# Kernel optimization log

Hardware: AMD Instinct MI355X
Metric: run time of the kernel (lower is better)

The kernel has to match this reference:

```python
import jax, jax.numpy as jnp
import numpy as np

SLOW = 32      # LSTM hidden size per weight-neuron
MSG = 16       # message size
MICRO = 2      # micro ticks per layer per step
LAYERS = [(256, 128), (128, 64)]
OUT_IDX = 0
EPS = 1e-6


def _lstm(x, h, c, Wi, Wh, b):
    g = x @ Wi + h @ Wh + b
    i, f, gg, o = jnp.split(g, 4, axis=-1)
    c = jax.nn.sigmoid(f) * c + jax.nn.sigmoid(i) * jnp.tanh(gg)
    h = jax.nn.sigmoid(o) * jnp.tanh(c)
    return h, c


def _ln(x, s, b):
    m = x.mean(-1, keepdims=True)
    v = ((x - m) ** 2).mean(-1, keepdims=True)
    return (x - m) * jax.lax.rsqrt(v + EPS) * s + b


def _merge(state):
    # mean-reduce first half of channels over batch, broadcast back
    half = state.shape[-1] // 2
    s1, s2 = state[..., :half], state[..., half:]
    s1 = jnp.broadcast_to(s1.mean(axis=0, keepdims=True), s1.shape)
    return jnp.concatenate([s1, s2], axis=-1)


def setup_inputs() -> dict:
    key = jax.random.key(0)
    ks = jax.random.split(key, 8)
    T, B = 4, 8
    sc = 0.1
    return {
        "inputs": jax.random.normal(ks[0], (T, B, LAYERS[0][0]), jnp.float32),
        "labels": jax.random.randint(ks[1], (T, B), 0, LAYERS[-1][1]),
        "Wi": jax.random.normal(ks[2], (2 * MSG, 4 * SLOW), jnp.float32) * sc,
        "Wh": jax.random.normal(ks[3], (SLOW, 4 * SLOW), jnp.float32) * sc,
        "b_lstm": jnp.zeros((4 * SLOW,), jnp.float32),
        "Wf": jax.random.normal(ks[4], (SLOW, MSG), jnp.float32) * sc,
        "bf": jnp.zeros((MSG,), jnp.float32),
        "Wb": jax.random.normal(ks[5], (SLOW, MSG), jnp.float32) * sc,
        "bwb": jnp.zeros((MSG,), jnp.float32),
        "ln_fs": jnp.ones((MSG,), jnp.float32),
        "ln_fb": jnp.zeros((MSG,), jnp.float32),
        "ln_bs": jnp.ones((MSG,), jnp.float32),
        "ln_bb": jnp.zeros((MSG,), jnp.float32),
    }


def reference(inputs, labels, Wi, Wh, b_lstm, Wf, bf, Wb, bwb,
              ln_fs, ln_fb, ln_bs, ln_bb):
    T, B, _ = inputs.shape
    n_out = LAYERS[-1][1]
    onehot = jax.nn.one_hot(labels, n_out, dtype=inputs.dtype)

    hs0 = tuple(jnp.zeros((B, i, o, SLOW), inputs.dtype) for i, o in LAYERS)
    cs0 = tuple(jnp.zeros((B, i, o, SLOW), inputs.dtype) for i, o in LAYERS)
    fwd0 = tuple(jnp.zeros((B, i, MSG), inputs.dtype) for i, o in LAYERS)
    bwd0 = tuple(jnp.zeros((B, o, MSG), inputs.dtype) for i, o in LAYERS)
    err0 = jnp.zeros((B, n_out, 2), inputs.dtype)

    def layer(h, c, f, bd):
        # h,c: (B,i,o,S); f: (B,i,M); bd: (B,o,M)
        Bq, ni, no, _ = h.shape
        x = jnp.concatenate([
            jnp.broadcast_to(f[:, :, None, :], (Bq, ni, no, MSG)),
            jnp.broadcast_to(bd[:, None, :, :], (Bq, ni, no, MSG)),
        ], axis=-1)  # (B,i,o,2M)
        for _ in range(MICRO):
            h, c = _lstm(x, h, c, Wi, Wh, b_lstm)
        fm = _ln(h @ Wf + bf, ln_fs, ln_fb)   # (B,i,o,M)
        bm = _ln(h @ Wb + bwb, ln_bs, ln_bb)  # (B,i,o,M)
        return h, c, fm.mean(axis=1), bm.mean(axis=2)

    def step(carry, x):
        hs, cs, fwd, bwd, error = carry
        inp, oh = x
        hs = [_merge(h) for h in hs]
        cs = [_merge(c) for c in cs]
        fwd = list(fwd)
        bwd = list(bwd)
        # inject input into channel 0 of first layer fwd msg
        fwd[0] = jnp.pad(inp[..., None], ((0, 0), (0, 0), (0, MSG - 1)))
        # inject 2-channel error into last layer bwd msg
        bwd[-1] = jnp.pad(error, ((0, 0), (0, 0), (0, MSG - 2)))
        out = None
        for i in range(len(LAYERS)):
            h, c, nf, nb = layer(hs[i], cs[i], fwd[i], bwd[i])
            hs[i], cs[i] = h, c
            if i > 0:
                bwd[i - 1] = nb.reshape(bwd[i - 1].shape)
            if i < len(LAYERS) - 1:
                fwd[i + 1] = nf.reshape(fwd[i + 1].shape)
            else:
                out = nf[..., OUT_IDX]  # (B, n_out)
        grad = jax.nn.softmax(out, axis=-1) - oh  # cross-entropy grad
        new_error = jnp.stack([grad, oh], axis=-1)  # feed_label=True
        return (tuple(hs), tuple(cs), tuple(fwd), tuple(bwd), new_error), out

    carry = (hs0, cs0, fwd0, bwd0, err0)
    _, outputs = jax.lax.scan(step, carry, (inputs, onehot))
    return outputs  # (T, B, n_out)
```

## Files before the change

kernel.cpp:

```cpp
#include <hip/hip_runtime.h>
#include <hip/hip_bf16.h>

#define SLOW 32
#define MSG 16
#define TSTEPS 4
#define BATCH 8
#define NI0 256
#define NO0 128
#define NI1 128
#define NO1 64

typedef __bf16 bf16x8 __attribute__((ext_vector_type(8)));
typedef float f32x4 __attribute__((ext_vector_type(4)));

__device__ __forceinline__ float rcpf(float x) { return __builtin_amdgcn_rcpf(x); }
__device__ __forceinline__ float sigf(float x) { return rcpf(1.f + __expf(-x)); }
__device__ __forceinline__ float tanh_apx(float x) {
    float xc = fminf(fmaxf(x, -15.f), 15.f);
    float e = __expf(-2.f * xc);
    return (1.f - e) * rcpf(1.f + e);
}
__device__ __forceinline__ unsigned short f2bf(float x) {
    __bf16 h = (__bf16)x;
    return __builtin_bit_cast(unsigned short, h);
}
__device__ __forceinline__ float bf2f(unsigned short u) {
    __bf16 h = __builtin_bit_cast(__bf16, u);
    return (float)h;
}
__device__ __forceinline__ float sum16(float v) {
    v += __shfl_xor(v, 1); v += __shfl_xor(v, 2);
    v += __shfl_xor(v, 4); v += __shfl_xor(v, 8);
    return v;
}

__global__ void k_prep(const float* __restrict__ Wh, const float* __restrict__ Wf,
                       const float* __restrict__ Wb, const float* __restrict__ Wi,
                       unsigned short* __restrict__ WhBp,
                       unsigned short* __restrict__ WfBp,
                       unsigned short* __restrict__ WbBp,
                       unsigned short* __restrict__ WiFp) {
    int i = blockIdx.x * 256 + threadIdx.x;
    if (i < 4096) {
        int e = i & 7, l = (i >> 3) & 63, nt = i >> 9;
        int k = (l >> 4) * 8 + e, col = nt * 16 + (l & 15);
        WhBp[i] = f2bf(Wh[k * 128 + col]);
    } else if (i < 4608) {
        int j = i - 4096;
        int e = j & 7, l = j >> 3;
        int k = (l >> 4) * 8 + e;
        WfBp[j] = f2bf(Wf[k * 16 + (l & 15)]);
    } else if (i < 5120) {
        int j = i - 4608;
        int e = j & 7, l = j >> 3;
        int k = (l >> 4) * 8 + e;
        WbBp[j] = f2bf(Wb[k * 16 + (l & 15)]);
    } else if (i < 9216) {
        int j = i - 5120;
        int e = j & 7, l = (j >> 3) & 63, nt = j >> 9;
        int k = (l >> 4) * 8 + e, col = nt * 16 + (l & 15);
        WiFp[j] = (k < 16) ? f2bf(Wi[k * 128 + col]) : (unsigned short)0;
    }
}

__global__ __launch_bounds__(256) void k_l0(
    const float* __restrict__ inp, const float* __restrict__ Wi,
    const unsigned short* __restrict__ WhBp, const float* __restrict__ b_lstm,
    const unsigned short* __restrict__ WfBp, const float* __restrict__ bf_,
    const float* __restrict__ ln_fs, const float* __restrict__ ln_fb,
    unsigned short* __restrict__ h0bf, float* __restrict__ c0g,
    const float* __restrict__ nb1, float* __restrict__ nf_part, int t) {
    int q = blockIdx.x & 1;
    int no = (blockIdx.x >> 1) & 127;
    int b = blockIdx.x >> 8;
    int tid = threadIdx.x;
    int w = __builtin_amdgcn_readfirstlane(tid >> 6);
    int l = tid & 63, lo = l & 15, hg = l >> 4;
    const bool wb = (t < TSTEPS - 1);

    __shared__ unsigned short Hbf[128 * 40];
    __shared__ unsigned short BW[4096];
    __shared__ unsigned short BFr[512];
    __shared__ float gsh[128];
    __shared__ float mi_l[128];
    __shared__ float wi0[128];
    __shared__ float redn[4][16];

    {
        unsigned int* d = (unsigned int*)BW;
        const unsigned int* s = (const unsigned int*)WhBp;
#pragma unroll
        for (int i = tid; i < 2048; i += 256) d[i] = s[i];
        ((unsigned int*)BFr)[tid] = ((const unsigned int*)WfBp)[tid];
    }
    if (tid < 128) {
        float acc = b_lstm[tid];
        if (t > 0) {
            const float* nbr = nb1 + ((size_t)b * NO0 + no) * MSG;
#pragma unroll
            for (int m = 0; m < MSG; m++) acc += nbr[m] * Wi[(MSG + m) * 128 + tid];
        }
        gsh[tid] = acc;
        wi0[tid] = Wi[tid];
        mi_l[tid] = inp[((size_t)t * BATCH + b) * NI0 + q * 128 + tid];
    }
    {
        int lc = tid >> 1, half = tid & 1;
        unsigned int* hl = (unsigned int*)Hbf;
        if (t > 0) {
            const unsigned int* hsrc =
                (const unsigned int*)h0bf +
                ((size_t)(b * NO0 + no) * 256 + q * 128 + lc) * 16 + half * 8;
#pragma unroll
            for (int j = 0; j < 8; j++) hl[lc * 20 + half * 8 + j] = hsrc[j];
        } else {
#pragma unroll
            for (int j = 0; j < 8; j++) hl[lc * 20 + half * 8 + j] = 0u;
        }
    }
    size_t cbase = (size_t)(b * NO0 + no) * 256 * 32;
    float cst[2][4][2];
    if (t > 0) {
#pragma unroll
        for (int mi_ = 0; mi_ < 2; mi_++)
#pragma unroll
            for (int r = 0; r < 4; r++) {
                int gc = q * 128 + (w * 2 + mi_) * 16 + hg * 4 + r;
#pragma unroll
                for (int hi = 0; hi < 2; hi++)
                    cst[mi_][r][hi] = c0g[cbase + (size_t)gc * 32 + lo + 16 * hi];
            }
    } else {
#pragma unroll
        for (int mi_ = 0; mi_ < 2; mi_++)
#pragma unroll
            for (int r = 0; r < 4; r++) { cst[mi_][r][0] = 0.f; cst[mi_][r][1] = 0.f; }
    }
    __syncthreads();

    float g8[8], w8[8];
#pragma unroll
    for (int nt = 0; nt < 8; nt++) { g8[nt] = gsh[lo + 16 * nt]; w8[nt] = wi0[lo + 16 * nt]; }
    f32x4 miv[2];
#pragma unroll
    for (int mi_ = 0; mi_ < 2; mi_++)
#pragma unroll
        for (int r = 0; r < 4; r++)
            miv[mi_][r] = mi_l[(w * 2 + mi_) * 16 + hg * 4 + r];

#pragma unroll
    for (int micro = 0; micro < 2; micro++) {
#pragma unroll
        for (int mi_ = 0; mi_ < 2; mi_++) {
            int lt = w * 2 + mi_;
            bf16x8 A = *(const bf16x8*)&Hbf[(lt * 16 + lo) * 40 + hg * 8];
            f32x4 acc[4];
#pragma unroll
            for (int g = 0; g < 4; g++) {
                int nt = 2 * g;
                bf16x8 B = *(const bf16x8*)&BW[(nt * 64 + l) * 8];
                f32x4 ci = g8[nt] + miv[mi_] * w8[nt];
                acc[g] = __builtin_amdgcn_mfma_f32_16x16x32_bf16(A, B, ci, 0, 0, 0);
            }
#pragma unroll
            for (int r = 0; r < 4; r++) {
                int lrow = lt * 16 + hg * 4 + r;
                float cn = sigf(acc[1][r]) * cst[mi_][r][0] + sigf(acc[0][r]) * tanh_apx(acc[2][r]);
                cst[mi_][r][0] = cn;
                float hv = sigf(acc[3][r]) * tanh_apx(cn);
                Hbf[lrow * 40 + lo] = f2bf(hv);
                if (micro == 1 && wb)
                    c0g[cbase + (size_t)(q * 128 + lrow) * 32 + lo] = cn;
            }
#pragma unroll
            for (int g = 0; g < 4; g++) {
                int nt = 2 * g + 1;
                bf16x8 B = *(const bf16x8*)&BW[(nt * 64 + l) * 8];
                f32x4 ci = g8[nt] + miv[mi_] * w8[nt];
                acc[g] = __builtin_amdgcn_mfma_f32_16x16x32_bf16(A, B, ci, 0, 0, 0);
            }
#pragma unroll
            for (int r = 0; r < 4; r++) {
                int lrow = lt * 16 + hg * 4 + r;
                float cn = sigf(acc[1][r]) * cst[mi_][r][1] + sigf(acc[0][r]) * tanh_apx(acc[2][r]);
                cst[mi_][r][1] = cn;
                float hv = sigf(acc[3][r]) * tanh_apx(cn);
                Hbf[lrow * 40 + lo + 16] = f2bf(hv);
                if (micro == 1 && wb)
                    c0g[cbase + (size_t)(q * 128 + lrow) * 32 + lo + 16] = cn;
            }
        }
    }

    bf16x8 Ff = *(const bf16x8*)&BFr[l * 8];
    float lnfs = ln_fs[lo], lnfb = ln_fb[lo];
    float bfv = bf_[lo];
    f32x4 cif = {bfv, bfv, bfv, bfv};
    float nfp = 0.f;
#pragma unroll
    for (int mi_ = 0; mi_ < 2; mi_++) {
        int lt = w * 2 + mi_;
        bf16x8 A = *(const bf16x8*)&Hbf[(lt * 16 + lo) * 40 + hg * 8];
        f32x4 f = __builtin_amdgcn_mfma_f32_16x16x32_bf16(A, Ff, cif, 0, 0, 0);
#pragma unroll
        for (int r = 0; r < 4; r++) {
            float x = f[r];
            float mean = sum16(x) * 0.0625f;
            float d = x - mean;
            float rs = rsqrtf(sum16(d * d) * 0.0625f + 1e-6f);
            nfp += d * rs * lnfs + lnfb;
        }
    }
    nfp += __shfl_xor(nfp, 16);
    nfp += __shfl_xor(nfp, 32);
    if (l < 16) redn[w][l] = nfp;
    __syncthreads();
    if (tid < 16)
        nf_part[(((size_t)b * NO0 + no) * 2 + q) * 16 + tid] =
            redn[0][tid] + redn[1][tid] + redn[2][tid] + redn[3][tid];

    if (wb) {
        int lc = tid >> 1, part = tid & 1;
        unsigned int* hdst =
            (unsigned int*)h0bf +
            ((size_t)(b * NO0 + no) * 256 + q * 128 + lc) * 16 + part * 8;
        const unsigned int* hl = (const unsigned int*)Hbf;
#pragma unroll
        for (int j = 0; j < 8; j++) hdst[j] = hl[lc * 20 + part * 8 + j];
    }
}

__global__ __launch_bounds__(256) void k_l1(
    const float* __restrict__ Wi, const unsigned short* __restrict__ WhBp,
    const float* __restrict__ b_lstm,
    const unsigned short* __restrict__ WfBp, const float* __restrict__ bf_,
    const float* __restrict__ ln_fs, const float* __restrict__ ln_fb,
    const unsigned short* __restrict__ WbBp, const float* __restrict__ bwb,
    const float* __restrict__ ln_bs, const float* __restrict__ ln_bb,
    const unsigned short* __restrict__ WiFp,
    unsigned short* __restrict__ h1bf, float* __restrict__ c1g,
    const float* __restrict__ nf_part, const float* __restrict__ gradP,
    const float* __restrict__ ohP,
    float* __restrict__ bm_g, float* __restrict__ outsum_part, int t) {
    int q = blockIdx.x & 1;
    int no = (blockIdx.x >> 1) & 63;
    int b = blockIdx.x >> 7;
    int tid = threadIdx.x;
    int w = __builtin_amdgcn_readfirstlane(tid >> 6);
    int l = tid & 63, lo = l & 15, hg = l >> 4;
    const bool wb = (t < TSTEPS - 1);

    __shared__ unsigned short Hbf[64 * 40];
    __shared__ unsigned short BW[4096];
    __shared__ unsigned short WiF[4096];
    __shared__ unsigned short BFr[512];
    __shared__ unsigned short BBr[512];
    __shared__ float gsh[128];
    __shared__ float red[4];

    {
        unsigned int* d = (unsigned int*)BW;
        const unsigned int* s = (const unsigned int*)WhBp;
        unsigned int* d2 = (unsigned int*)WiF;
        const unsigned int* s2 = (const unsigned int*)WiFp;
#pragma unroll
        for (int i = tid; i < 2048; i += 256) { d[i] = s[i]; d2[i] = s2[i]; }
        ((unsigned int*)BFr)[tid] = ((const unsigned int*)WfBp)[tid];
        ((unsigned int*)BBr)[tid] = ((const unsigned int*)WbBp)[tid];
    }
    if (tid < 128) {
        float acc = b_lstm[tid];
        if (t > 0) {
            float g = gradP[b * NO1 + no], oh = ohP[b * NO1 + no];
            acc += g * Wi[MSG * 128 + tid] + oh * Wi[(MSG + 1) * 128 + tid];
        }
        gsh[tid] = acc;
    }
    {
        int lc = tid >> 2, part = tid & 3;
        unsigned int* hl = (unsigned int*)Hbf;
        if (t > 0) {
            const unsigned int* hsrc =
                (const unsigned int*)h1bf +
                ((size_t)(b * NO1 + no) * 128 + q * 64 + lc) * 16 + part * 4;
#pragma unroll
            for (int j = 0; j < 4; j++) hl[lc * 20 + part * 4 + j] = hsrc[j];
        } else {
#pragma unroll
            for (int j = 0; j < 4; j++) hl[lc * 20 + part * 4 + j] = 0u;
        }
    }
    size_t cbase = (size_t)(b * NO1 + no) * 128 * 32;
    float cst[4][2];
    if (t > 0) {
#pragma unroll
        for (int r = 0; r < 4; r++) {
            int gc = q * 64 + w * 16 + hg * 4 + r;
#pragma unroll
            for (int hi = 0; hi < 2; hi++)
                cst[r][hi] = c1g[cbase + (size_t)gc * 32 + lo + 16 * hi];
        }
    } else {
#pragma unroll
        for (int r = 0; r < 4; r++) { cst[r][0] = 0.f; cst[r][1] = 0.f; }
    }
    bf16x8 Anf;
#pragma unroll
    for (int e = 0; e < 8; e++) Anf[e] = (__bf16)0.f;
    if (hg < 2) {
        const float* p = nf_part +
            ((size_t)b * 128 + q * 64 + w * 16 + lo) * 32 + hg * 8;
#pragma unroll
        for (int e = 0; e < 8; e++)
            Anf[e] = (__bf16)((p[e] + p[e + 16]) * (1.f / 256.f));
    }
    __syncthreads();

    f32x4 xf4[8];
    {
        f32x4 zz = {0.f, 0.f, 0.f, 0.f};
#pragma unroll
        for (int nt = 0; nt < 8; nt++) {
            bf16x8 B = *(const bf16x8*)&WiF[(nt * 64 + l) * 8];
            xf4[nt] = __builtin_amdgcn_mfma_f32_16x16x32_bf16(Anf, B, zz, 0, 0, 0);
        }
    }
    float g8[8];
#pragma unroll
    for (int nt = 0; nt < 8; nt++) g8[nt] = gsh[lo + 16 * nt];

#pragma unroll
    for (int micro = 0; micro < 2; micro++) {
        bf16x8 A = *(const bf16x8*)&Hbf[(w * 16 + lo) * 40 + hg * 8];
        f32x4 acc[4];
#pragma unroll
        for (int g = 0; g < 4; g++) {
            int nt = 2 * g;
            bf16x8 B = *(const bf16x8*)&BW[(nt * 64 + l) * 8];
            f32x4 ci = xf4[nt] + g8[nt];
            acc[g] = __builtin_amdgcn_mfma_f32_16x16x32_bf16(A, B, ci, 0, 0, 0);
        }
#pragma unroll
        for (int r = 0; r < 4; r++) {
            float cn = sigf(acc[1][r]) * cst[r][0] + sigf(acc[0][r]) * tanh_apx(acc[2][r]);
            cst[r][0] = cn;
            float hv = sigf(acc[3][r]) * tanh_apx(cn);
            Hbf[(w * 16 + hg * 4 + r) * 40 + lo] = f2bf(hv);
            if (micro == 1 && wb)
                c1g[cbase + (size_t)(q * 64 + w * 16 + hg * 4 + r) * 32 + lo] = cn;
        }
#pragma unroll
        for (int g = 0; g < 4; g++) {
            int nt = 2 * g + 1;
            bf16x8 B = *(const bf16x8*)&BW[(nt * 64 + l) * 8];
            f32x4 ci = xf4[nt] + g8[nt];
            acc[g] = __builtin_amdgcn_mfma_f32_16x16x32_bf16(A, B, ci, 0, 0, 0);
        }
#pragma unroll
        for (int r = 0; r < 4; r++) {
            float cn = sigf(acc[1][r]) * cst[r][1] + sigf(acc[0][r]) * tanh_apx(acc[2][r]);
            cst[r][1] = cn;
            float hv = sigf(acc[3][r]) * tanh_apx(cn);
            Hbf[(w * 16 + hg * 4 + r) * 40 + lo + 16] = f2bf(hv);
            if (micro == 1 && wb)
                c1g[cbase + (size_t)(q * 64 + w * 16 + hg * 4 + r) * 32 + lo + 16] = cn;
        }
    }

    bf16x8 Ff = *(const bf16x8*)&BFr[l * 8];
    float lnfs = ln_fs[lo], lnfb = ln_fb[lo];
    float bfv = bf_[lo];
    f32x4 cif = {bfv, bfv, bfv, bfv};
    float op = 0.f;
    {
        bf16x8 A = *(const bf16x8*)&Hbf[(w * 16 + lo) * 40 + hg * 8];
        f32x4 f = __builtin_amdgcn_mfma_f32_16x16x32_bf16(A, Ff, cif, 0, 0, 0);
#pragma unroll
        for (int r = 0; r < 4; r++) {
            float x = f[r];
            float mean = sum16(x) * 0.0625f;
            float d = x - mean;
            float rs = rsqrtf(sum16(d * d) * 0.0625f + 1e-6f);
            op += d * rs * lnfs + lnfb;
        }
        if (wb) {
            bf16x8 Bb = *(const bf16x8*)&BBr[l * 8];
            float lnbs = ln_bs[lo], lnbb = ln_bb[lo];
            float bwv = bwb[lo];
            f32x4 cib = {bwv, bwv, bwv, bwv};
            f32x4 g = __builtin_amdgcn_mfma_f32_16x16x32_bf16(A, Bb, cib, 0, 0, 0);
#pragma unroll
            for (int r = 0; r < 4; r++) {
                int gc = q * 64 + w * 16 + hg * 4 + r;
                float x = g[r];
                float mean = sum16(x) * 0.0625f;
                float d = x - mean;
                float rs = rsqrtf(sum16(d * d) * 0.0625f + 1e-6f);
                bm_g[(((size_t)b * NO1 + no) * MSG + lo) * NI1 + gc] = d * rs * lnbs + lnbb;
            }
        }
    }
    op += __shfl_xor(op, 16);
    op += __shfl_xor(op, 32);
    if (l == 0) red[w] = op;
    __syncthreads();
    if (tid == 0)
        outsum_part[((size_t)b * NO1 + no) * 2 + q] = red[0] + red[1] + red[2] + red[3];

    if (wb) {
        int lc = tid >> 2, part = tid & 3;
        unsigned int* hdst =
            (unsigned int*)h1bf +
            ((size_t)(b * NO1 + no) * 128 + q * 64 + lc) * 16 + part * 4;
        const unsigned int* hl = (const unsigned int*)Hbf;
#pragma unroll
        for (int j = 0; j < 4; j++) hdst[j] = hl[lc * 20 + part * 4 + j];
    }
}

__global__ __launch_bounds__(256) void k_step_end(
    unsigned int* __restrict__ h0, float* __restrict__ c0,
    unsigned int* __restrict__ h1, float* __restrict__ c1,
    const float* __restrict__ bm_g, float* __restrict__ nb1,
    const float* __restrict__ outsum_part, const int* __restrict__ labels,
    float* __restrict__ dout, float* __restrict__ gradP,
    float* __restrict__ ohP, int t) {
    int bid = blockIdx.x;
    if (bid < 1920) {
        int idx = bid * 256 + threadIdx.x;
        if (idx < 262144) {
            int u = idx & 7, cell = (idx >> 3) & 255, no = idx >> 11;
            size_t base = ((size_t)no * 256 + cell) * 16 + u;
            const size_t strd = (size_t)128 * 256 * 16;
            float s0 = 0.f, s1 = 0.f;
#pragma unroll
            for (int b = 0; b < 8; b++) {
                unsigned int v = h0[base + b * strd];
                s0 += bf2f((unsigned short)(v & 0xffff));
                s1 += bf2f((unsigned short)(v >> 16));
            }
            unsigned int mv = (unsigned int)f2bf(s0 * 0.125f) |
                              ((unsigned int)f2bf(s1 * 0.125f) << 16);
#pragma unroll
            for (int b = 0; b < 8; b++) h0[base + b * strd] = mv;
            return;
        }
        idx -= 262144;
        if (idx < 131072) {
            int s4 = idx & 3, cell = (idx >> 2) & 255, no = idx >> 10;
            float4* C = (float4*)c0;
            size_t base = ((size_t)no * 256 + cell) * 8 + s4;
            const size_t strd = (size_t)128 * 256 * 8;
            float4 a = {0.f, 0.f, 0.f, 0.f};
#pragma unroll
            for (int b = 0; b < 8; b++) {
                float4 v = C[base + b * strd];
                a.x += v.x; a.y += v.y; a.z += v.z; a.w += v.w;
            }
            a.x *= 0.125f; a.y *= 0.125f; a.z *= 0.125f; a.w *= 0.125f;
#pragma unroll
            for (int b = 0; b < 8; b++) C[base + b * strd] = a;
            return;
        }
        idx -= 131072;
        if (idx < 65536) {
            int u = idx & 7, cell = (idx >> 3) & 127, no = idx >> 10;
            size_t base = ((size_t)no * 128 + cell) * 16 + u;
            const size_t strd = (size_t)64 * 128 * 16;
            float s0 = 0.f, s1 = 0.f;
#pragma unroll
            for (int b = 0; b < 8; b++) {
                unsigned int v = h1[base + b * strd];
                s0 += bf2f((unsigned short)(v & 0xffff));
                s1 += bf2f((unsigned short)(v >> 16));
            }
            unsigned int mv = (unsigned int)f2bf(s0 * 0.125f) |
                              ((unsigned int)f2bf(s1 * 0.125f) << 16);
#pragma unroll
            for (int b = 0; b < 8; b++) h1[base + b * strd] = mv;
            return;
        }
        idx -= 65536;
        {
            int s4 = idx & 3, cell = (idx >> 2) & 127, no = idx >> 9;
            float4* C = (float4*)c1;
            size_t base = ((size_t)no * 128 + cell) * 8 + s4;
            const size_t strd = (size_t)64 * 128 * 8;
            float4 a = {0.f, 0.f, 0.f, 0.f};
#pragma unroll
            for (int b = 0; b < 8; b++) {
                float4 v = C[base + b * strd];
                a.x += v.x; a.y += v.y; a.z += v.z; a.w += v.w;
            }
            a.x *= 0.125f; a.y *= 0.125f; a.z *= 0.125f; a.w *= 0.125f;
#pragma unroll
            for (int b = 0; b < 8; b++) C[base + b * strd] = a;
        }
        return;
    }
    if (bid < 1984) {
        int g = (bid - 1920) * 256 + threadIdx.x;
        int ni = g & 127;
        int m = (g >> 7) & 15;
        int b = g >> 11;
        float a = 0.f;
#pragma unroll 8
        for (int no = 0; no < NO1; no++)
            a += bm_g[(((size_t)b * NO1 + no) * MSG + m) * NI1 + ni];
        nb1[((size_t)b * NI1 + ni) * MSG + m] = a * (1.f / NO1);
        return;
    }
    {
        int b = bid - 1984;
        int no = threadIdx.x;
        if (no < 64) {
            float v = (outsum_part[((size_t)b * NO1 + no) * 2] +
                       outsum_part[((size_t)b * NO1 + no) * 2 + 1]) * (1.f / 128.f);
            float mx = v;
#pragma unroll
            for (int d = 1; d < 64; d <<= 1) mx = fmaxf(mx, __shfl_xor(mx, d));
            float e = __expf(v - mx);
            float sum = e;
#pragma unroll
            for (int d = 1; d < 64; d <<= 1) sum += __shfl_xor(sum, d);
            int lbl = labels[t * BATCH + b];
            float oh = (no == lbl) ? 1.f : 0.f;
            gradP[b * NO1 + no] = e / sum - oh;
            ohP[b * NO1 + no] = oh;
            dout[((size_t)t * BATCH + b) * NO1 + no] = v;
        }
    }
}

__global__ void k_fin(const float* __restrict__ outsum_part,
                      float* __restrict__ dout) {
    int b = blockIdx.x;
    int no = threadIdx.x;
    float v = (outsum_part[((size_t)b * NO1 + no) * 2] +
               outsum_part[((size_t)b * NO1 + no) * 2 + 1]) * (1.f / 128.f);
    dout[((size_t)(TSTEPS - 1) * BATCH + b) * NO1 + no] = v;
}


extern "C" void kernel_launch(void* const* d_in, const int* in_sizes, int n_in,
                              void* d_out, int out_size, void* d_ws, size_t ws_size,
                              hipStream_t stream) {
    const float* inp   = (const float*)d_in[0];
    const int*   labels= (const int*)d_in[1];
    const float* Wi    = (const float*)d_in[2];
    const float* Wh    = (const float*)d_in[3];
    const float* b_lstm= (const float*)d_in[4];
    const float* Wf    = (const float*)d_in[5];
    const float* bf_   = (const float*)d_in[6];
    const float* Wb    = (const float*)d_in[7];
    const float* bwb   = (const float*)d_in[8];
    const float* ln_fs = (const float*)d_in[9];
    const float* ln_fb = (const float*)d_in[10];
    const float* ln_bs = (const float*)d_in[11];
    const float* ln_bb = (const float*)d_in[12];
    float* out = (float*)d_out;

    const size_t SZ0 = (size_t)BATCH * NO0 * 256 * 32;
    const size_t SZ1 = (size_t)BATCH * NO1 * 128 * 32;

    float* c0 = (float*)d_ws;
    float* c1 = c0 + SZ0;
    unsigned short* h0bf = (unsigned short*)(c1 + SZ1);
    unsigned short* h1bf = h0bf + SZ0;
    float* bm_g        = (float*)(h1bf + SZ1);
    float* nf_part     = bm_g + 1048576;
    float* nb1         = nf_part + 32768;
    float* outsum_part = nb1 + 16384;
    float* gradP       = outsum_part + 1024;
    float* ohP         = gradP + 512;
    unsigned short* WhBp = (unsigned short*)(ohP + 512);
    unsigned short* WfBp = WhBp + 4096;
    unsigned short* WbBp = WfBp + 512;
    unsigned short* WiFp = WbBp + 512;

    k_prep<<<36, 256, 0, stream>>>(Wh, Wf, Wb, Wi, WhBp, WfBp, WbBp, WiFp);

    for (int t = 0; t < TSTEPS; t++) {
        k_l0<<<BATCH * NO0 * 2, 256, 0, stream>>>(inp, Wi, WhBp, b_lstm, WfBp, bf_,
                                                  ln_fs, ln_fb, h0bf, c0, nb1,
                                                  nf_part, t);
        k_l1<<<BATCH * NO1 * 2, 256, 0, stream>>>(Wi, WhBp, b_lstm, WfBp, bf_,
                                                  ln_fs, ln_fb, WbBp, bwb, ln_bs, ln_bb,
                                                  WiFp, h1bf, c1, nf_part, gradP, ohP,
                                                  bm_g, outsum_part, t);
        if (t < TSTEPS - 1) {
            k_step_end<<<1992, 256, 0, stream>>>((unsigned int*)h0bf, c0,
                                                 (unsigned int*)h1bf, c1,
                                                 bm_g, nb1, outsum_part, labels,
                                                 out, gradP, ohP, t);
        } else {
            k_fin<<<BATCH, 64, 0, stream>>>(outsum_part, out);
        }
    }
}
```

Measured before the change: 279.6 us.

## Store batch-mean state compactly and fold layer-0 merge into layer-1 launch

The batch-mean merge no longer broadcasts averaged h/c back into all 8 batch copies. It writes a compact per-neuron mean buffer (hm/cm), which the LSTM kernels read for the first half of channels. The layer-0 merge reductions also move into extra blocks of the k_l1 launch, so they overlap with layer-1 compute and shrink k_step_end. This cuts the write-back traffic of the full state tensors, at the cost of extra workspace and a larger k_l1 grid.

```diff
diff --git a/kernel.cpp b/kernel.cpp
--- a/kernel.cpp
+++ b/kernel.cpp
@@ -69,6 +69,7 @@
     const unsigned short* __restrict__ WfBp, const float* __restrict__ bf_,
     const float* __restrict__ ln_fs, const float* __restrict__ ln_fb,
     unsigned short* __restrict__ h0bf, float* __restrict__ c0g,
+    const unsigned short* __restrict__ hm0, const float* __restrict__ cm0,
     const float* __restrict__ nb1, float* __restrict__ nf_part, int t) {
     int q = blockIdx.x & 1;
     int no = (blockIdx.x >> 1) & 127;
@@ -108,11 +109,17 @@
         int lc = tid >> 1, half = tid & 1;
         unsigned int* hl = (unsigned int*)Hbf;
         if (t > 0) {
-            const unsigned int* hsrc =
-                (const unsigned int*)h0bf +
-                ((size_t)(b * NO0 + no) * 256 + q * 128 + lc) * 16 + half * 8;
-#pragma unroll
-            for (int j = 0; j < 8; j++) hl[lc * 20 + half * 8 + j] = hsrc[j];
+            if (half == 0) {
+                const unsigned int* hsrc = (const unsigned int*)hm0 +
+                    ((size_t)no * 256 + q * 128 + lc) * 8;
+#pragma unroll
+                for (int j = 0; j < 8; j++) hl[lc * 20 + j] = hsrc[j];
+            } else {
+                const unsigned int* hsrc = (const unsigned int*)h0bf +
+                    ((size_t)(b * NO0 + no) * 256 + q * 128 + lc) * 16 + 8;
+#pragma unroll
+                for (int j = 0; j < 8; j++) hl[lc * 20 + 8 + j] = hsrc[j];
+            }
         } else {
 #pragma unroll
             for (int j = 0; j < 8; j++) hl[lc * 20 + half * 8 + j] = 0u;
@@ -126,9 +133,8 @@
 #pragma unroll
             for (int r = 0; r < 4; r++) {
                 int gc = q * 128 + (w * 2 + mi_) * 16 + hg * 4 + r;
-#pragma unroll
-                for (int hi = 0; hi < 2; hi++)
-                    cst[mi_][r][hi] = c0g[cbase + (size_t)gc * 32 + lo + 16 * hi];
+                cst[mi_][r][0] = cm0[((size_t)no * 256 + gc) * 16 + lo];
+                cst[mi_][r][1] = c0g[cbase + (size_t)gc * 32 + lo + 16];
             }
     } else {
 #pragma unroll
@@ -239,13 +245,51 @@
     const float* __restrict__ ln_bs, const float* __restrict__ ln_bb,
     const unsigned short* __restrict__ WiFp,
     unsigned short* __restrict__ h1bf, float* __restrict__ c1g,
+    const unsigned short* __restrict__ hm1, const float* __restrict__ cm1,
+    const unsigned short* __restrict__ h0bf, const float* __restrict__ c0g,
+    unsigned short* __restrict__ hm0, float* __restrict__ cm0,
     const float* __restrict__ nf_part, const float* __restrict__ gradP,
     const float* __restrict__ ohP,
     float* __restrict__ bm_g, float* __restrict__ outsum_part, int t) {
+    int tid = threadIdx.x;
+    if (blockIdx.x >= 1024) {
+        int mb = blockIdx.x - 1024;
+        if (mb < 1024) {
+            int idx = mb * 256 + tid;
+            int u = idx & 7, cell = (idx >> 3) & 255, no = idx >> 11;
+            size_t base = ((size_t)no * 256 + cell) * 16 + u;
+            const size_t strd = (size_t)NO0 * 256 * 16;
+            const unsigned int* H = (const unsigned int*)h0bf;
+            float s0 = 0.f, s1 = 0.f;
+#pragma unroll
+            for (int b = 0; b < 8; b++) {
+                unsigned int v = H[base + b * strd];
+                s0 += bf2f((unsigned short)(v & 0xffff));
+                s1 += bf2f((unsigned short)(v >> 16));
+            }
+            ((unsigned int*)hm0)[((size_t)no * 256 + cell) * 8 + u] =
+                (unsigned int)f2bf(s0 * 0.125f) | ((unsigned int)f2bf(s1 * 0.125f) << 16);
+        } else {
+            int idx = (mb - 1024) * 256 + tid;
+            int s4 = idx & 3, cell = (idx >> 2) & 255, no = idx >> 10;
+            const float4* C = (const float4*)c0g;
+            size_t base = ((size_t)no * 256 + cell) * 8 + s4;
+            const size_t strd = (size_t)NO0 * 256 * 8;
+            float4 a = {0.f, 0.f, 0.f, 0.f};
+#pragma unroll
+            for (int b = 0; b < 8; b++) {
+                float4 v = C[base + b * strd];
+                a.x += v.x; a.y += v.y; a.z += v.z; a.w += v.w;
+            }
+            a.x *= 0.125f; a.y *= 0.125f; a.z *= 0.125f; a.w *= 0.125f;
+            ((float4*)cm0)[((size_t)no * 256 + cell) * 4 + s4] = a;
+        }
+        return;
+    }
+
     int q = blockIdx.x & 1;
     int no = (blockIdx.x >> 1) & 63;
     int b = blockIdx.x >> 7;
-    int tid = threadIdx.x;
     int w = __builtin_amdgcn_readfirstlane(tid >> 6);
     int l = tid & 63, lo = l & 15, hg = l >> 4;
     const bool wb = (t < TSTEPS - 1);
@@ -280,11 +324,17 @@
         int lc = tid >> 2, part = tid & 3;
         unsigned int* hl = (unsigned int*)Hbf;
         if (t > 0) {
-            const unsigned int* hsrc =
-                (const unsigned int*)h1bf +
-                ((size_t)(b * NO1 + no) * 128 + q * 64 + lc) * 16 + part * 4;
-#pragma unroll
-            for (int j = 0; j < 4; j++) hl[lc * 20 + part * 4 + j] = hsrc[j];
+            if (part < 2) {
+                const unsigned int* hsrc = (const unsigned int*)hm1 +
+                    ((size_t)no * 128 + q * 64 + lc) * 8 + part * 4;
+#pragma unroll
+                for (int j = 0; j < 4; j++) hl[lc * 20 + part * 4 + j] = hsrc[j];
+            } else {
+                const unsigned int* hsrc = (const unsigned int*)h1bf +
+                    ((size_t)(b * NO1 + no) * 128 + q * 64 + lc) * 16 + part * 4;
+#pragma unroll
+                for (int j = 0; j < 4; j++) hl[lc * 20 + part * 4 + j] = hsrc[j];
+            }
         } else {
 #pragma unroll
             for (int j = 0; j < 4; j++) hl[lc * 20 + part * 4 + j] = 0u;
@@ -296,9 +346,8 @@
 #pragma unroll
         for (int r = 0; r < 4; r++) {
             int gc = q * 64 + w * 16 + hg * 4 + r;
-#pragma unroll
-            for (int hi = 0; hi < 2; hi++)
-                cst[r][hi] = c1g[cbase + (size_t)gc * 32 + lo + 16 * hi];
+            cst[r][0] = cm1[((size_t)no * 128 + gc) * 16 + lo];
+            cst[r][1] = c1g[cbase + (size_t)gc * 32 + lo + 16];
         }
     } else {
 #pragma unroll
@@ -419,87 +468,47 @@
 }
 
 __global__ __launch_bounds__(256) void k_step_end(
-    unsigned int* __restrict__ h0, float* __restrict__ c0,
-    unsigned int* __restrict__ h1, float* __restrict__ c1,
+    const unsigned int* __restrict__ h1, const float* __restrict__ c1,
+    unsigned short* __restrict__ hm1, float* __restrict__ cm1,
     const float* __restrict__ bm_g, float* __restrict__ nb1,
     const float* __restrict__ outsum_part, const int* __restrict__ labels,
     float* __restrict__ dout, float* __restrict__ gradP,
     float* __restrict__ ohP, int t) {
     int bid = blockIdx.x;
-    if (bid < 1920) {
+    if (bid < 256) {
         int idx = bid * 256 + threadIdx.x;
-        if (idx < 262144) {
-            int u = idx & 7, cell = (idx >> 3) & 255, no = idx >> 11;
-            size_t base = ((size_t)no * 256 + cell) * 16 + u;
-            const size_t strd = (size_t)128 * 256 * 16;
-            float s0 = 0.f, s1 = 0.f;
-#pragma unroll
-            for (int b = 0; b < 8; b++) {
-                unsigned int v = h0[base + b * strd];
-                s0 += bf2f((unsigned short)(v & 0xffff));
-                s1 += bf2f((unsigned short)(v >> 16));
-            }
-            unsigned int mv = (unsigned int)f2bf(s0 * 0.125f) |
-                              ((unsigned int)f2bf(s1 * 0.125f) << 16);
-#pragma unroll
-            for (int b = 0; b < 8; b++) h0[base + b * strd] = mv;
-            return;
-        }
-        idx -= 262144;
-        if (idx < 131072) {
-            int s4 = idx & 3, cell = (idx >> 2) & 255, no = idx >> 10;
-            float4* C = (float4*)c0;
-            size_t base = ((size_t)no * 256 + cell) * 8 + s4;
-            const size_t strd = (size_t)128 * 256 * 8;
-            float4 a = {0.f, 0.f, 0.f, 0.f};
-#pragma unroll
-            for (int b = 0; b < 8; b++) {
-                float4 v = C[base + b * strd];
-                a.x += v.x; a.y += v.y; a.z += v.z; a.w += v.w;
-            }
-            a.x *= 0.125f; a.y *= 0.125f; a.z *= 0.125f; a.w *= 0.125f;
-#pragma unroll
-            for (int b = 0; b < 8; b++) C[base + b * strd] = a;
-            return;
-        }
-        idx -= 131072;
-        if (idx < 65536) {
-            int u = idx & 7, cell = (idx >> 3) & 127, no = idx >> 10;
-            size_t base = ((size_t)no * 128 + cell) * 16 + u;
-            const size_t strd = (size_t)64 * 128 * 16;
-            float s0 = 0.f, s1 = 0.f;
-#pragma unroll
-            for (int b = 0; b < 8; b++) {
-                unsigned int v = h1[base + b * strd];
-                s0 += bf2f((unsigned short)(v & 0xffff));
-                s1 += bf2f((unsigned short)(v >> 16));
-            }
-            unsigned int mv = (unsigned int)f2bf(s0 * 0.125f) |
-                              ((unsigned int)f2bf(s1 * 0.125f) << 16);
-#pragma unroll
-            for (int b = 0; b < 8; b++) h1[base + b * strd] = mv;
-            return;
-        }
-        idx -= 65536;
-        {
-            int s4 = idx & 3, cell = (idx >> 2) & 127, no = idx >> 9;
-            float4* C = (float4*)c1;
-            size_t base = ((size_t)no * 128 + cell) * 8 + s4;
-            const size_t strd = (size_t)64 * 128 * 8;
-            float4 a = {0.f, 0.f, 0.f, 0.f};
-#pragma unroll
-            for (int b = 0; b < 8; b++) {
-                float4 v = C[base + b * strd];
-                a.x += v.x; a.y += v.y; a.z += v.z; a.w += v.w;
-            }
-            a.x *= 0.125f; a.y *= 0.125f; a.z *= 0.125f; a.w *= 0.125f;
-#pragma unroll
-            for (int b = 0; b < 8; b++) C[base + b * strd] = a;
-        }
+        int u = idx & 7, cell = (idx >> 3) & 127, no = idx >> 10;
+        size_t base = ((size_t)no * 128 + cell) * 16 + u;
+        const size_t strd = (size_t)NO1 * 128 * 16;
+        float s0 = 0.f, s1 = 0.f;
+#pragma unroll
+        for (int b = 0; b < 8; b++) {
+            unsigned int v = h1[base + b * strd];
+            s0 += bf2f((unsigned short)(v & 0xffff));
+            s1 += bf2f((unsigned short)(v >> 16));
+        }
+        ((unsigned int*)hm1)[((size_t)no * 128 + cell) * 8 + u] =
+            (unsigned int)f2bf(s0 * 0.125f) | ((unsigned int)f2bf(s1 * 0.125f) << 16);
         return;
     }
-    if (bid < 1984) {
-        int g = (bid - 1920) * 256 + threadIdx.x;
+    if (bid < 384) {
+        int idx = (bid - 256) * 256 + threadIdx.x;
+        int s4 = idx & 3, cell = (idx >> 2) & 127, no = idx >> 9;
+        const float4* C = (const float4*)c1;
+        size_t base = ((size_t)no * 128 + cell) * 8 + s4;
+        const size_t strd = (size_t)NO1 * 128 * 8;
+        float4 a = {0.f, 0.f, 0.f, 0.f};
+#pragma unroll
+        for (int b = 0; b < 8; b++) {
+            float4 v = C[base + b * strd];
+            a.x += v.x; a.y += v.y; a.z += v.z; a.w += v.w;
+        }
+        a.x *= 0.125f; a.y *= 0.125f; a.z *= 0.125f; a.w *= 0.125f;
+        ((float4*)cm1)[((size_t)no * 128 + cell) * 4 + s4] = a;
+        return;
+    }
+    if (bid < 448) {
+        int g = (bid - 384) * 256 + threadIdx.x;
         int ni = g & 127;
         int m = (g >> 7) & 15;
         int b = g >> 11;
@@ -511,7 +520,7 @@
         return;
     }
     {
-        int b = bid - 1984;
+        int b = bid - 448;
         int no = threadIdx.x;
         if (no < 64) {
             float v = (outsum_part[((size_t)b * NO1 + no) * 2] +
@@ -567,7 +576,11 @@
     float* c1 = c0 + SZ0;
     unsigned short* h0bf = (unsigned short*)(c1 + SZ1);
     unsigned short* h1bf = h0bf + SZ0;
-    float* bm_g        = (float*)(h1bf + SZ1);
+    float* cm0         = (float*)(h1bf + SZ1);
+    float* cm1         = cm0 + 524288;
+    unsigned short* hm0 = (unsigned short*)(cm1 + 131072);
+    unsigned short* hm1 = hm0 + 524288;
+    float* bm_g        = (float*)(hm1 + 131072);
     float* nf_part     = bm_g + 1048576;
     float* nb1         = nf_part + 32768;
     float* outsum_part = nb1 + 16384;
@@ -582,17 +595,19 @@
 
     for (int t = 0; t < TSTEPS; t++) {
         k_l0<<<BATCH * NO0 * 2, 256, 0, stream>>>(inp, Wi, WhBp, b_lstm, WfBp, bf_,
-                                                  ln_fs, ln_fb, h0bf, c0, nb1,
-                                                  nf_part, t);
-        k_l1<<<BATCH * NO1 * 2, 256, 0, stream>>>(Wi, WhBp, b_lstm, WfBp, bf_,
-                                                  ln_fs, ln_fb, WbBp, bwb, ln_bs, ln_bb,
-                                                  WiFp, h1bf, c1, nf_part, gradP, ohP,
-                                                  bm_g, outsum_part, t);
+                                                  ln_fs, ln_fb, h0bf, c0, hm0, cm0,
+                                                  nb1, nf_part, t);
+        int l1grid = (t < TSTEPS - 1) ? 2560 : 1024;
+        k_l1<<<l1grid, 256, 0, stream>>>(Wi, WhBp, b_lstm, WfBp, bf_,
+                                         ln_fs, ln_fb, WbBp, bwb, ln_bs, ln_bb,
+                                         WiFp, h1bf, c1, hm1, cm1,
+                                         h0bf, c0, hm0, cm0,
+                                         nf_part, gradP, ohP,
+                                         bm_g, outsum_part, t);
         if (t < TSTEPS - 1) {
-            k_step_end<<<1992, 256, 0, stream>>>((unsigned int*)h0bf, c0,
-                                                 (unsigned int*)h1bf, c1,
-                                                 bm_g, nb1, outsum_part, labels,
-                                                 out, gradP, ohP, t);
+            k_step_end<<<456, 256, 0, stream>>>((const unsigned int*)h1bf, c1,
+                                                hm1, cm1, bm_g, nb1, outsum_part,
+                                                labels, out, gradP, ohP, t);
         } else {
             k_fin<<<BATCH, 64, 0, stream>>>(outsum_part, out);
         }
```

After: 253.6 us. -9.3%, faster.
